# Kernel optimization log

Hardware: AMD Instinct MI355X
Metric: run time of the kernel (lower is better)

The kernel has to match this reference:

```python
import jax, jax.numpy as jnp
import numpy as np

NUM_EMBEDDINGS = 4096
EMBED_DIM = 256
BETA = 0.25


def setup_inputs() -> dict:
    key = jax.random.key(0)
    kz, ke = jax.random.split(key)
    z = jax.random.normal(kz, (16, 4096, EMBED_DIM), dtype=jnp.float32)
    lim = 1.0 / NUM_EMBEDDINGS
    emb = jax.random.uniform(ke, (NUM_EMBEDDINGS, EMBED_DIM), dtype=jnp.float32,
                             minval=-lim, maxval=lim)
    return {"z": z, "emb": emb}


def reference(z, emb):
    B, T, D = z.shape
    flat_z = z.reshape(-1, D)                                  # [N, D]
    # squared euclidean distances via ||z||^2 - 2 z.e^T + ||e||^2
    dist = (jnp.sum(flat_z ** 2, axis=1, keepdims=True)
            - 2.0 * flat_z @ emb.T
            + jnp.sum(emb ** 2, axis=1))                       # [N, K]
    indices = jnp.argmin(dist, axis=1)                         # [N]
    z_q = emb[indices].reshape(z.shape)                        # [B, T, D]
    sg = jax.lax.stop_gradient
    codebook_loss = jnp.mean((sg(z_q) - z) ** 2)
    commit_loss = jnp.mean((z_q - sg(z)) ** 2)
    loss = codebook_loss + BETA * commit_loss
    z_q_st = z + sg(z_q - z)                                   # straight-through
    return z_q_st, loss, indices.reshape(B, T)
```

## Files before the change

kernel.cpp:

```cpp
#include <hip/hip_runtime.h>

#define N_ROWS 65536
#define K_CODES 4096
#define D_DIM 256
#define MARGIN_BF 6.0e-5f
#define CAP_DUEL 24576
#define CAP_FULL 8192

typedef __attribute__((ext_vector_type(8))) _Float16 f16x8;
typedef __attribute__((ext_vector_type(4))) float f32x4;

typedef __attribute__((address_space(1))) unsigned int g_u32;
typedef __attribute__((address_space(3))) unsigned int l_u32;
#define GLOAD16(gp, lp) __builtin_amdgcn_global_load_lds((g_u32*)(gp), (l_u32*)(lp), 16, 0, 0)


union f16u { _Float16 h; unsigned short u; };

static __device__ __forceinline__ unsigned int pack2(float a, float b) {
    f16u x, y; x.h = (_Float16)a; y.h = (_Float16)b;
    return (unsigned)x.u | ((unsigned)y.u << 16);
}

static __device__ __forceinline__ void norm_body(const float* __restrict__ src,
                                                 float* __restrict__ dst, int bi, int tid) {
    int row = bi * 64 + (tid >> 2);
    int q = tid & 3;
    const float* p = src + (size_t)row * D_DIM;
    double acc = 0.0;
#pragma unroll 4
    for (int it = 0; it < 16; ++it) {
        float4 v = *(const float4*)&p[(q + 4 * it) * 4];
        float a = v.x * v.x, b = v.y * v.y, c = v.z * v.z, d = v.w * v.w;
        acc += (double)a; acc += (double)b; acc += (double)c; acc += (double)d;
    }
    acc += __shfl_xor(acc, 1);
    acc += __shfl_xor(acc, 2);
    if (q == 0) dst[row] = (float)acc;
}

__global__ __launch_bounds__(256) void cvt_emb_kernel(const float* __restrict__ emb,
                                                      unsigned short* __restrict__ emb_perm,
                                                      float* __restrict__ cvec,
                                                      int* __restrict__ cnts) {
    if (blockIdx.x >= 512) {
        if (blockIdx.x == 512 && threadIdx.x < 2) cnts[threadIdx.x] = 0;
        norm_body(emb, cvec, blockIdx.x - 512, threadIdx.x);
        return;
    }
    int gid = blockIdx.x * 256 + threadIdx.x;
    int lane = gid & 63;
    int f = gid >> 6;
    int cf = f & 1;
    int d8 = (f >> 1) & 7;
    int step = (f >> 4) & 63;
    int h = f >> 10;
    int code = h * 2048 + step * 32 + cf * 16 + (lane & 15);
    int d0 = d8 * 32 + (lane >> 4) * 8;
    const float* p = emb + (size_t)code * D_DIM + d0;
    float4 v0 = *(const float4*)p;
    float4 v1 = *(const float4*)(p + 4);
    uint4 o;
    o.x = pack2(v0.x * 4096.0f, v0.y * 4096.0f);
    o.y = pack2(v0.z * 4096.0f, v0.w * 4096.0f);
    o.z = pack2(v1.x * 4096.0f, v1.y * 4096.0f);
    o.w = pack2(v1.z * 4096.0f, v1.w * 4096.0f);
    *(uint4*)((char*)emb_perm + (size_t)gid * 16) = o;
}

__global__ __launch_bounds__(256) void cvt_z_kernel(const float* __restrict__ z,
                                                    unsigned short* __restrict__ z_perm,
                                                    float* __restrict__ rownorm,
                                                    unsigned long long* __restrict__ rescored) {
    if (blockIdx.x >= 8192) {
        norm_body(z, rownorm, blockIdx.x - 8192, threadIdx.x);
        return;
    }
    if (blockIdx.x < 256) rescored[blockIdx.x * 256 + threadIdx.x] = ~0ull;
    int ft = blockIdx.x * 256 + threadIdx.x;
    int lane = ft & 63;
    int rf = (ft >> 6) & 3;
    int d8 = (ft >> 8) & 7;
    int rg = ft >> 11;
    int row = rg * 64 + rf * 16 + (lane & 15);
    int d0 = d8 * 32 + (lane >> 4) * 8;
    const float* p = z + (size_t)row * D_DIM + d0;
    float4 v0 = *(const float4*)p;
    float4 v1 = *(const float4*)(p + 4);
    uint4 o;
    o.x = pack2(v0.x, v0.y);
    o.y = pack2(v0.z, v0.w);
    o.z = pack2(v1.x, v1.y);
    o.w = pack2(v1.z, v1.w);
    *(uint4*)((char*)z_perm + (size_t)ft * 16) = o;
}

__global__ __launch_bounds__(256, 2) void phaseB_kernel(
        const unsigned short* __restrict__ z_perm, const unsigned short* __restrict__ emb_perm,
        const float* __restrict__ cvec, float* __restrict__ out_idx,
        int* __restrict__ cnts, int* __restrict__ fulllist,
        unsigned long long* __restrict__ duellist) {
    __shared__ float cv[4096];
    __shared__ unsigned short ring[2][8][1024];

    const int tid = threadIdx.x;
    const int lane = tid & 63;
    const int w = tid >> 6;
    const int pp = w >> 1;
    const int h = w & 1;
    const int l15 = lane & 15, l4 = lane >> 4;
    const int rb = blockIdx.x;

#pragma unroll
    for (int i = 0; i < 4; ++i) {
        int idx = i * 1024 + tid * 4;
        *(float4*)&cv[idx] = *(const float4*)&cvec[idx];
    }

    f16x8 A[8][4];
    {
        const char* zsrc = (const char*)z_perm + (size_t)(rb * 2 + pp) * 32768 + lane * 16;
#pragma unroll
        for (int d8 = 0; d8 < 8; ++d8)
#pragma unroll
            for (int rf = 0; rf < 4; ++rf)
                A[d8][rf] = *(const f16x8*)(zsrc + (d8 * 4 + rf) * 1024);
    }
    __syncthreads();

    const char* bsrc = (const char*)emb_perm + (size_t)h * 1048576 + pp * 1024 + lane * 16;
    char* ldst = (char*)&ring[h][0][0] + pp * 1024;
    const char* lrd = (const char*)&ring[h][0][0] + lane * 16;

#pragma unroll
    for (int q = 0; q < 6; ++q)
        GLOAD16(bsrc + q * 2048, ldst + q * 2048);
    asm volatile("s_waitcnt vmcnt(5)" ::: "memory");
    __builtin_amdgcn_s_barrier();
    __builtin_amdgcn_sched_barrier(0);

    f16x8 B0a = *(const f16x8*)(lrd);
    f16x8 B0b = *(const f16x8*)(lrd + 1024);
    f16x8 B1a, B1b;

    float m1[16], m2[16], m3[16];
#pragma unroll
    for (int t = 0; t < 16; ++t) { m1[t] = 3.4e38f; m2[t] = 3.4e38f; m3[t] = 3.4e38f; }

    f32x4 acc[4][2];

    for (int step = 0; step < 64; ++step) {
        const int kb = h * 2048 + step * 32;
        float ck0 = cv[kb + l15];
        float ck1 = cv[kb + 16 + l15];
#pragma unroll
        for (int rf = 0; rf < 4; ++rf) {
            acc[rf][0] = (f32x4){0.f, 0.f, 0.f, 0.f};
            acc[rf][1] = (f32x4){0.f, 0.f, 0.f, 0.f};
        }
#pragma unroll
        for (int d8 = 0; d8 < 8; ++d8) {
            {
                const char* g = bsrc + (size_t)(step * 8 + d8 + 6) * 2048
                                - ((step == 63 && d8 >= 2) ? 1048576 : 0);
                GLOAD16(g, ldst + ((d8 + 6) & 7) * 2048);
            }
            asm volatile("s_waitcnt vmcnt(5)" ::: "memory");
            __builtin_amdgcn_s_barrier();
            __builtin_amdgcn_sched_barrier(0);
            {
                const char* rp = lrd + ((d8 + 1) & 7) * 2048;
                if ((d8 + 1) & 1) { B1a = *(const f16x8*)rp; B1b = *(const f16x8*)(rp + 1024); }
                else              { B0a = *(const f16x8*)rp; B0b = *(const f16x8*)(rp + 1024); }
            }
            f16x8 b0 = (d8 & 1) ? B1a : B0a;
            f16x8 b1 = (d8 & 1) ? B1b : B0b;
#pragma unroll
            for (int rf = 0; rf < 4; ++rf) {
                acc[rf][0] = __builtin_amdgcn_mfma_f32_16x16x32_f16(A[d8][rf], b0, acc[rf][0], 0, 0, 0);
                acc[rf][1] = __builtin_amdgcn_mfma_f32_16x16x32_f16(A[d8][rf], b1, acc[rf][1], 0, 0, 0);
            }
        }

#pragma unroll
        for (int cf = 0; cf < 2; ++cf) {
            const float ck = cf ? ck1 : ck0;
            const unsigned cg = (unsigned)(kb + cf * 16 + l15);
#pragma unroll
            for (int rf = 0; rf < 4; ++rf)
#pragma unroll
                for (int j = 0; j < 4; ++j) {
                    float d = fmaf(-4.8828125e-4f, acc[rf][cf][j], ck);
                    float dp = __uint_as_float((__float_as_uint(d) & 0xfffff000u) | cg);
                    const int t = rf * 4 + j;
                    m3[t] = __builtin_amdgcn_fmed3f(dp, m2[t], m3[t]);
                    m2[t] = __builtin_amdgcn_fmed3f(dp, m1[t], m2[t]);
                    m1[t] = fminf(m1[t], dp);
                }
        }
    }

    __syncthreads();
    float* m1s = cv;
    float* m2s = cv + 256;
    float* m3s = cv + 512;
#pragma unroll
    for (int t = 0; t < 16; ++t) {
        float a1 = m1[t], a2 = m2[t], a3 = m3[t];
        for (int msk = 8; msk >= 1; msk >>= 1) {
            float b1 = __shfl_xor(a1, msk);
            float b2 = __shfl_xor(a2, msk);
            float b3 = __shfl_xor(a3, msk);
            bool bw = b1 < a1;
            float w1 = bw ? b1 : a1, w2 = bw ? b2 : a2, w3 = bw ? b3 : a3;
            float l1 = bw ? a1 : b1, l2 = bw ? a2 : b2;
            bool t2 = l1 < w2;
            a1 = w1;
            a2 = t2 ? l1 : w2;
            a3 = t2 ? fminf(w2, l2) : fminf(w3, l1);
        }
        if (l15 == 0) {
            int rloc = (t >> 2) * 16 + l4 * 4 + (t & 3);
            m1s[w * 64 + rloc] = a1;
            m2s[w * 64 + rloc] = a2;
            m3s[w * 64 + rloc] = a3;
        }
    }
    __syncthreads();

    if (tid < 128) {
        int pg = tid >> 6, r = tid & 63;
        int wA = pg * 2, wB = pg * 2 + 1;
        float a1 = m1s[wA * 64 + r], a2 = m2s[wA * 64 + r], a3 = m3s[wA * 64 + r];
        float b1 = m1s[wB * 64 + r], b2 = m2s[wB * 64 + r], b3 = m3s[wB * 64 + r];
        bool bw = b1 < a1;
        float w1 = bw ? b1 : a1, w2 = bw ? b2 : a2, w3 = bw ? b3 : a3;
        float l1 = bw ? a1 : b1, l2 = bw ? a2 : b2;
        bool t2 = l1 < w2;
        float f1 = w1;
        float f2 = t2 ? l1 : w2;
        float f3 = t2 ? fminf(w2, l2) : fminf(w3, l1);

        int i1 = (int)(__float_as_uint(f1) & 0xfffu);
        int i2 = (int)(__float_as_uint(f2) & 0xfffu);
        int rowg = rb * 128 + pg * 64 + r;
        out_idx[rowg] = (float)i1;
        if (f3 - f1 < MARGIN_BF) {
            int pz = atomicAdd(&cnts[1], 1);
            if (pz < CAP_FULL) fulllist[pz] = rowg;
        } else if (f2 - f1 < MARGIN_BF) {
            int pz = atomicAdd(&cnts[0], 1);
            if (pz < CAP_DUEL) {
                duellist[pz] = ((unsigned long long)(unsigned)rowg << 32) |
                               ((unsigned)i1 << 16) | (unsigned)i2;
            } else {
                int pf = atomicAdd(&cnts[1], 1);
                if (pf < CAP_FULL) fulllist[pf] = rowg;
            }
        }
    }
}

__global__ __launch_bounds__(256) void duel_kernel(
        const float* __restrict__ z, const float* __restrict__ emb,
        const float* __restrict__ rownorm, const float* __restrict__ cvec,
        const int* __restrict__ cnts, const unsigned long long* __restrict__ duellist,
        unsigned long long* __restrict__ rescored) {
    int n = cnts[0];
    if (n > CAP_DUEL) n = CAP_DUEL;
    for (int i = blockIdx.x * 256 + threadIdx.x; i < n; i += 64 * 256) {
        unsigned long long e = duellist[i];
        int row = (int)(e >> 32);
        int c1 = (int)((e >> 16) & 0xfffu);
        int c2 = (int)(e & 0xfffu);
        const float* zp = z + (size_t)row * D_DIM;
        const float* p1 = emb + (size_t)c1 * D_DIM;
        const float* p2 = emb + (size_t)c2 * D_DIM;
        float a1 = 0.f, a2 = 0.f;
#pragma unroll 8
        for (int d4 = 0; d4 < 64; ++d4) {
            float4 zf = *(const float4*)&zp[d4 * 4];
            float4 e1 = *(const float4*)&p1[d4 * 4];
            float4 e2 = *(const float4*)&p2[d4 * 4];
            a1 = fmaf(zf.x, e1.x, a1); a1 = fmaf(zf.y, e1.y, a1);
            a1 = fmaf(zf.z, e1.z, a1); a1 = fmaf(zf.w, e1.w, a1);
            a2 = fmaf(zf.x, e2.x, a2); a2 = fmaf(zf.y, e2.y, a2);
            a2 = fmaf(zf.z, e2.z, a2); a2 = fmaf(zf.w, e2.w, a2);
        }
        float rn = rownorm[row];
        float d1 = __fadd_rn(__fsub_rn(rn, __fmul_rn(2.0f, a1)), cvec[c1]);
        float d2 = __fadd_rn(__fsub_rn(rn, __fmul_rn(2.0f, a2)), cvec[c2]);
        unsigned long long p1v = ((unsigned long long)__float_as_uint(d1) << 32) | (unsigned)c1;
        unsigned long long p2v = ((unsigned long long)__float_as_uint(d2) << 32) | (unsigned)c2;
        rescored[row] = p1v < p2v ? p1v : p2v;
    }
}

__global__ __launch_bounds__(256) void rescore_kernel(
        const float* __restrict__ z, const float* __restrict__ emb,
        const float* __restrict__ rownorm, const float* __restrict__ cvec,
        const int* __restrict__ cnts, const int* __restrict__ fulllist,
        unsigned long long* __restrict__ rescored) {
    __shared__ float zs[16][256];
    __shared__ float sa[16];
    __shared__ int srow[16];
    const int tid = threadIdx.x;
    int cnt = cnts[1];
    if (cnt > CAP_FULL) cnt = CAP_FULL;
    const int nu = ((cnt + 15) >> 4) << 2;
    for (int uu = blockIdx.x; uu < nu; uu += gridDim.x) {
        int rg = uu >> 2, ks = uu & 3;
        __syncthreads();
        if (tid < 16) {
            int fi = rg * 16 + tid;
            int row = fulllist[fi < cnt ? fi : 0];
            srow[tid] = row;
            sa[tid] = rownorm[row];
        }
        __syncthreads();
#pragma unroll
        for (int i = 0; i < 4; ++i) {
            int u = i * 256 + tid;
            int r = u >> 6, d4 = u & 63;
            *(float4*)&zs[r][d4 * 4] = *(const float4*)&z[(size_t)srow[r] * D_DIM + d4 * 4];
        }
        __syncthreads();

        const int c0 = ks * 1024 + tid;
        float acc[16][4];
#pragma unroll
        for (int r = 0; r < 16; ++r)
#pragma unroll
            for (int j = 0; j < 4; ++j) acc[r][j] = 0.f;

        for (int ch = 0; ch < 8; ++ch) {
#pragma unroll
            for (int q = 0; q < 8; ++q) {
                float4 e0 = *(const float4*)&emb[(size_t)(c0      ) * D_DIM + ch * 32 + q * 4];
                float4 e1 = *(const float4*)&emb[(size_t)(c0 + 256) * D_DIM + ch * 32 + q * 4];
                float4 e2 = *(const float4*)&emb[(size_t)(c0 + 512) * D_DIM + ch * 32 + q * 4];
                float4 e3 = *(const float4*)&emb[(size_t)(c0 + 768) * D_DIM + ch * 32 + q * 4];
#pragma unroll
                for (int r = 0; r < 16; ++r) {
                    float4 zf = *(const float4*)&zs[r][ch * 32 + q * 4];
                    acc[r][0] = fmaf(zf.x, e0.x, acc[r][0]);
                    acc[r][0] = fmaf(zf.y, e0.y, acc[r][0]);
                    acc[r][0] = fmaf(zf.z, e0.z, acc[r][0]);
                    acc[r][0] = fmaf(zf.w, e0.w, acc[r][0]);
                    acc[r][1] = fmaf(zf.x, e1.x, acc[r][1]);
                    acc[r][1] = fmaf(zf.y, e1.y, acc[r][1]);
                    acc[r][1] = fmaf(zf.z, e1.z, acc[r][1]);
                    acc[r][1] = fmaf(zf.w, e1.w, acc[r][1]);
                    acc[r][2] = fmaf(zf.x, e2.x, acc[r][2]);
                    acc[r][2] = fmaf(zf.y, e2.y, acc[r][2]);
                    acc[r][2] = fmaf(zf.z, e2.z, acc[r][2]);
                    acc[r][2] = fmaf(zf.w, e2.w, acc[r][2]);
                    acc[r][3] = fmaf(zf.x, e3.x, acc[r][3]);
                    acc[r][3] = fmaf(zf.y, e3.y, acc[r][3]);
                    acc[r][3] = fmaf(zf.z, e3.z, acc[r][3]);
                    acc[r][3] = fmaf(zf.w, e3.w, acc[r][3]);
                }
            }
        }
        const float ck0 = cvec[c0], ck1 = cvec[c0 + 256];
        const float ck2 = cvec[c0 + 512], ck3 = cvec[c0 + 768];
#pragma unroll
        for (int r = 0; r < 16; ++r) {
            float d0 = __fadd_rn(__fsub_rn(sa[r], __fmul_rn(2.0f, acc[r][0])), ck0);
            float d1 = __fadd_rn(__fsub_rn(sa[r], __fmul_rn(2.0f, acc[r][1])), ck1);
            float d2 = __fadd_rn(__fsub_rn(sa[r], __fmul_rn(2.0f, acc[r][2])), ck2);
            float d3 = __fadd_rn(__fsub_rn(sa[r], __fmul_rn(2.0f, acc[r][3])), ck3);
            unsigned long long p0 = ((unsigned long long)__float_as_uint(d0) << 32) | (unsigned)(c0);
            unsigned long long p1 = ((unsigned long long)__float_as_uint(d1) << 32) | (unsigned)(c0 + 256);
            unsigned long long p2 = ((unsigned long long)__float_as_uint(d2) << 32) | (unsigned)(c0 + 512);
            unsigned long long p3 = ((unsigned long long)__float_as_uint(d3) << 32) | (unsigned)(c0 + 768);
            unsigned long long pa = p0 < p1 ? p0 : p1;
            unsigned long long pb = p2 < p3 ? p2 : p3;
            unsigned long long pm = pa < pb ? pa : pb;
            for (int msk = 32; msk >= 1; msk >>= 1) {
                unsigned long long qv = __shfl_xor(pm, msk);
                pm = qv < pm ? qv : pm;
            }
            if ((tid & 63) == 0) atomicMin(&rescored[srow[r]], pm);
        }
    }
}

__global__ __launch_bounds__(256) void writeback_kernel(
        const float* __restrict__ z, const float* __restrict__ emb,
        const unsigned long long* __restrict__ rescored,
        float* __restrict__ out_idx, float* __restrict__ out0,
        double* __restrict__ partials) {
    const int tid = threadIdx.x;
    const int base = blockIdx.x * 32;
    double acc = 0.0;
    for (int g = 0; g < 8; ++g) {
        int row = base + g * 4 + (tid >> 6);
        int d4 = tid & 63;
        unsigned long long rv = rescored[row];
        int idx;
        if (rv != ~0ull) {
            idx = (int)(unsigned)(rv & 0xffffffffull);
            if (d4 == 0) out_idx[row] = (float)idx;
        } else {
            idx = (int)out_idx[row];
        }
        float4 q4 = *(const float4*)&emb[(size_t)idx * D_DIM + d4 * 4];
        float4 z4 = *(const float4*)&z[(size_t)row * D_DIM + d4 * 4];
        float4 o;
        float dx;
        dx = q4.x - z4.x; o.x = z4.x + dx; acc += (double)dx * dx;
        dx = q4.y - z4.y; o.y = z4.y + dx; acc += (double)dx * dx;
        dx = q4.z - z4.z; o.z = z4.z + dx; acc += (double)dx * dx;
        dx = q4.w - z4.w; o.w = z4.w + dx; acc += (double)dx * dx;
        *(float4*)&out0[(size_t)row * D_DIM + d4 * 4] = o;
    }
    for (int m = 32; m >= 1; m >>= 1) acc += __shfl_xor(acc, m);
    __shared__ double sd[4];
    if ((tid & 63) == 0) sd[tid >> 6] = acc;
    __syncthreads();
    if (tid == 0) partials[blockIdx.x] = (sd[0] + sd[1]) + (sd[2] + sd[3]);
}

__global__ void finalize_kernel(const double* __restrict__ partials, float* __restrict__ out_loss) {
    __shared__ double sd[256];
    const int tid = threadIdx.x;
    double a = 0.0;
    for (int i = tid; i < 2048; i += 256) a += partials[i];
    sd[tid] = a;
    __syncthreads();
    for (int s = 128; s > 0; s >>= 1) {
        if (tid < s) sd[tid] += sd[tid + s];
        __syncthreads();
    }
    if (tid == 0) {
        double m = sd[0] / 16777216.0;
        out_loss[0] = (float)(m + 0.25 * m);
    }
}

extern "C" void kernel_launch(void* const* d_in, const int* in_sizes, int n_in,
                              void* d_out, int out_size, void* d_ws, size_t ws_size,
                              hipStream_t stream) {
    const float* z = (const float*)d_in[0];
    const float* emb = (const float*)d_in[1];
    float* out0 = (float*)d_out;
    float* out_loss = out0 + (size_t)N_ROWS * D_DIM;
    float* out_idx = out_loss + 1;

    char* ws = (char*)d_ws;
    float* rownorm = (float*)ws;
    float* cvec = (float*)(ws + 262144);
    unsigned short* emb_perm = (unsigned short*)(ws + 278528);
    int* cnts = (int*)(ws + 2375680);
    int* fulllist = (int*)(ws + 2375936);
    unsigned long long* duellist = (unsigned long long*)(ws + 2408704);
    unsigned long long* rescored = (unsigned long long*)(ws + 2605312);
    double* partials = (double*)(ws + 3129600);

    unsigned short* z_perm = (unsigned short*)d_out;

    cvt_emb_kernel<<<576, 256, 0, stream>>>(emb, emb_perm, cvec, cnts);
    cvt_z_kernel<<<9216, 256, 0, stream>>>(z, z_perm, rownorm, rescored);
    phaseB_kernel<<<512, 256, 0, stream>>>(z_perm, emb_perm, cvec, out_idx, cnts, fulllist, duellist);
    rescore_kernel<<<256, 256, 0, stream>>>(z, emb, rownorm, cvec, cnts, fulllist, rescored);
    duel_kernel<<<64, 256, 0, stream>>>(z, emb, rownorm, cvec, cnts, duellist, rescored);
    writeback_kernel<<<N_ROWS / 32, 256, 0, stream>>>(z, emb, rescored, out_idx, out0, partials);
    finalize_kernel<<<1, 256, 0, stream>>>(partials, out_loss);
}
```

Baseline: 296.1 us.

## Fuse z fp16 conversion into phaseB and compute row norms on demand

Removes the separate cvt_z kernel, which wrote a permuted fp16 copy of z and computed every row norm. phaseB now reads fp32 z directly and packs it to fp16 in registers. Row norms are recomputed only for the rows that need rescoring, inside the duel and rescore kernels. This drops a full pass over z (read 64MB, write 32MB) and a kernel launch. In exchange phaseB reads twice as many bytes with less coalesced strided loads, and the duel kernel does extra double-precision work.

```diff
diff --git a/kernel.cpp b/kernel.cpp
--- a/kernel.cpp
+++ b/kernel.cpp
@@ -42,12 +42,14 @@
 __global__ __launch_bounds__(256) void cvt_emb_kernel(const float* __restrict__ emb,
                                                       unsigned short* __restrict__ emb_perm,
                                                       float* __restrict__ cvec,
-                                                      int* __restrict__ cnts) {
+                                                      int* __restrict__ cnts,
+                                                      unsigned long long* __restrict__ rescored) {
     if (blockIdx.x >= 512) {
         if (blockIdx.x == 512 && threadIdx.x < 2) cnts[threadIdx.x] = 0;
         norm_body(emb, cvec, blockIdx.x - 512, threadIdx.x);
         return;
     }
+    if (blockIdx.x < 256) rescored[blockIdx.x * 256 + threadIdx.x] = ~0ull;
     int gid = blockIdx.x * 256 + threadIdx.x;
     int lane = gid & 63;
     int f = gid >> 6;
@@ -68,35 +70,8 @@
     *(uint4*)((char*)emb_perm + (size_t)gid * 16) = o;
 }
 
-__global__ __launch_bounds__(256) void cvt_z_kernel(const float* __restrict__ z,
-                                                    unsigned short* __restrict__ z_perm,
-                                                    float* __restrict__ rownorm,
-                                                    unsigned long long* __restrict__ rescored) {
-    if (blockIdx.x >= 8192) {
-        norm_body(z, rownorm, blockIdx.x - 8192, threadIdx.x);
-        return;
-    }
-    if (blockIdx.x < 256) rescored[blockIdx.x * 256 + threadIdx.x] = ~0ull;
-    int ft = blockIdx.x * 256 + threadIdx.x;
-    int lane = ft & 63;
-    int rf = (ft >> 6) & 3;
-    int d8 = (ft >> 8) & 7;
-    int rg = ft >> 11;
-    int row = rg * 64 + rf * 16 + (lane & 15);
-    int d0 = d8 * 32 + (lane >> 4) * 8;
-    const float* p = z + (size_t)row * D_DIM + d0;
-    float4 v0 = *(const float4*)p;
-    float4 v1 = *(const float4*)(p + 4);
-    uint4 o;
-    o.x = pack2(v0.x, v0.y);
-    o.y = pack2(v0.z, v0.w);
-    o.z = pack2(v1.x, v1.y);
-    o.w = pack2(v1.z, v1.w);
-    *(uint4*)((char*)z_perm + (size_t)ft * 16) = o;
-}
-
 __global__ __launch_bounds__(256, 2) void phaseB_kernel(
-        const unsigned short* __restrict__ z_perm, const unsigned short* __restrict__ emb_perm,
+        const float* __restrict__ z, const unsigned short* __restrict__ emb_perm,
         const float* __restrict__ cvec, float* __restrict__ out_idx,
         int* __restrict__ cnts, int* __restrict__ fulllist,
         unsigned long long* __restrict__ duellist) {
@@ -119,12 +94,21 @@
 
     f16x8 A[8][4];
     {
-        const char* zsrc = (const char*)z_perm + (size_t)(rb * 2 + pp) * 32768 + lane * 16;
+        union { f16x8 v; unsigned u[4]; } cvt;
+        const float* zr = z + ((size_t)(rb * 128 + pp * 64 + l15)) * D_DIM + l4 * 8;
 #pragma unroll
         for (int d8 = 0; d8 < 8; ++d8)
 #pragma unroll
-            for (int rf = 0; rf < 4; ++rf)
-                A[d8][rf] = *(const f16x8*)(zsrc + (d8 * 4 + rf) * 1024);
+            for (int rf = 0; rf < 4; ++rf) {
+                const float* p = zr + rf * 16 * D_DIM + d8 * 32;
+                float4 v0 = *(const float4*)p;
+                float4 v1 = *(const float4*)(p + 4);
+                cvt.u[0] = pack2(v0.x, v0.y);
+                cvt.u[1] = pack2(v0.z, v0.w);
+                cvt.u[2] = pack2(v1.x, v1.y);
+                cvt.u[3] = pack2(v1.z, v1.w);
+                A[d8][rf] = cvt.v;
+            }
     }
     __syncthreads();
 
@@ -263,7 +247,7 @@
 
 __global__ __launch_bounds__(256) void duel_kernel(
         const float* __restrict__ z, const float* __restrict__ emb,
-        const float* __restrict__ rownorm, const float* __restrict__ cvec,
+        const float* __restrict__ cvec,
         const int* __restrict__ cnts, const unsigned long long* __restrict__ duellist,
         unsigned long long* __restrict__ rescored) {
     int n = cnts[0];
@@ -277,6 +261,7 @@
         const float* p1 = emb + (size_t)c1 * D_DIM;
         const float* p2 = emb + (size_t)c2 * D_DIM;
         float a1 = 0.f, a2 = 0.f;
+        double n0 = 0.0, n1 = 0.0, n2 = 0.0, n3 = 0.0;
 #pragma unroll 8
         for (int d4 = 0; d4 < 64; ++d4) {
             float4 zf = *(const float4*)&zp[d4 * 4];
@@ -286,8 +271,15 @@
             a1 = fmaf(zf.z, e1.z, a1); a1 = fmaf(zf.w, e1.w, a1);
             a2 = fmaf(zf.x, e2.x, a2); a2 = fmaf(zf.y, e2.y, a2);
             a2 = fmaf(zf.z, e2.z, a2); a2 = fmaf(zf.w, e2.w, a2);
-        }
-        float rn = rownorm[row];
+            float sx = zf.x * zf.x, sy = zf.y * zf.y, sz = zf.z * zf.z, sw = zf.w * zf.w;
+            switch (d4 & 3) {
+                case 0: n0 += (double)sx; n0 += (double)sy; n0 += (double)sz; n0 += (double)sw; break;
+                case 1: n1 += (double)sx; n1 += (double)sy; n1 += (double)sz; n1 += (double)sw; break;
+                case 2: n2 += (double)sx; n2 += (double)sy; n2 += (double)sz; n2 += (double)sw; break;
+                default: n3 += (double)sx; n3 += (double)sy; n3 += (double)sz; n3 += (double)sw; break;
+            }
+        }
+        float rn = (float)((n0 + n1) + (n2 + n3));
         float d1 = __fadd_rn(__fsub_rn(rn, __fmul_rn(2.0f, a1)), cvec[c1]);
         float d2 = __fadd_rn(__fsub_rn(rn, __fmul_rn(2.0f, a2)), cvec[c2]);
         unsigned long long p1v = ((unsigned long long)__float_as_uint(d1) << 32) | (unsigned)c1;
@@ -298,7 +290,7 @@
 
 __global__ __launch_bounds__(256) void rescore_kernel(
         const float* __restrict__ z, const float* __restrict__ emb,
-        const float* __restrict__ rownorm, const float* __restrict__ cvec,
+        const float* __restrict__ cvec,
         const int* __restrict__ cnts, const int* __restrict__ fulllist,
         unsigned long long* __restrict__ rescored) {
     __shared__ float zs[16][256];
@@ -313,9 +305,7 @@
         __syncthreads();
         if (tid < 16) {
             int fi = rg * 16 + tid;
-            int row = fulllist[fi < cnt ? fi : 0];
-            srow[tid] = row;
-            sa[tid] = rownorm[row];
+            srow[tid] = fulllist[fi < cnt ? fi : 0];
         }
         __syncthreads();
 #pragma unroll
@@ -323,6 +313,20 @@
             int u = i * 256 + tid;
             int r = u >> 6, d4 = u & 63;
             *(float4*)&zs[r][d4 * 4] = *(const float4*)&z[(size_t)srow[r] * D_DIM + d4 * 4];
+        }
+        __syncthreads();
+        if (tid < 64) {
+            int r = tid >> 2, q = tid & 3;
+            double acc = 0.0;
+#pragma unroll 4
+            for (int it = 0; it < 16; ++it) {
+                float4 v = *(const float4*)&zs[r][(q + 4 * it) * 4];
+                float a = v.x * v.x, b = v.y * v.y, c = v.z * v.z, d = v.w * v.w;
+                acc += (double)a; acc += (double)b; acc += (double)c; acc += (double)d;
+            }
+            acc += __shfl_xor(acc, 1);
+            acc += __shfl_xor(acc, 2);
+            if (q == 0) sa[r] = (float)acc;
         }
         __syncthreads();
 
@@ -449,7 +453,6 @@
     float* out_idx = out_loss + 1;
 
     char* ws = (char*)d_ws;
-    float* rownorm = (float*)ws;
     float* cvec = (float*)(ws + 262144);
     unsigned short* emb_perm = (unsigned short*)(ws + 278528);
     int* cnts = (int*)(ws + 2375680);
@@ -458,13 +461,10 @@
     unsigned long long* rescored = (unsigned long long*)(ws + 2605312);
     double* partials = (double*)(ws + 3129600);
 
-    unsigned short* z_perm = (unsigned short*)d_out;
-
-    cvt_emb_kernel<<<576, 256, 0, stream>>>(emb, emb_perm, cvec, cnts);
-    cvt_z_kernel<<<9216, 256, 0, stream>>>(z, z_perm, rownorm, rescored);
-    phaseB_kernel<<<512, 256, 0, stream>>>(z_perm, emb_perm, cvec, out_idx, cnts, fulllist, duellist);
-    rescore_kernel<<<256, 256, 0, stream>>>(z, emb, rownorm, cvec, cnts, fulllist, rescored);
-    duel_kernel<<<64, 256, 0, stream>>>(z, emb, rownorm, cvec, cnts, duellist, rescored);
+    cvt_emb_kernel<<<576, 256, 0, stream>>>(emb, emb_perm, cvec, cnts, rescored);
+    phaseB_kernel<<<512, 256, 0, stream>>>(z, emb_perm, cvec, out_idx, cnts, fulllist, duellist);
+    rescore_kernel<<<256, 256, 0, stream>>>(z, emb, cvec, cnts, fulllist, rescored);
+    duel_kernel<<<64, 256, 0, stream>>>(z, emb, cvec, cnts, duellist, rescored);
     writeback_kernel<<<N_ROWS / 32, 256, 0, stream>>>(z, emb, rescored, out_idx, out0, partials);
     finalize_kernel<<<1, 256, 0, stream>>>(partials, out_loss);
 }
```

Result: no change. 293.3 us (-1.0%).
